# Kernel tuning notes

Measured on AMD Instinct MI355X. Metric: run time of the kernel, lower is better.

Reference implementation:

```python
import jax, jax.numpy as jnp
import numpy as np


def setup_inputs() -> dict:
    key = jax.random.key(0)
    k1, k2, k3, k4 = jax.random.split(key, 4)
    B, C, H, W = 4, 512, 64, 64
    K = 20
    Cp = C // 4  # 128, proj_feat output channels
    feat = jax.random.normal(k1, (B, C, H, W), dtype=jnp.float32)
    cam = jax.random.uniform(k2, (B, K, H, W), dtype=jnp.float32)
    # 1x1 conv == linear over channel dim; store kernel as [Cout, Cin]
    w_proj = jax.random.normal(k3, (Cp, C), dtype=jnp.float32) * (1.0 / np.sqrt(C))
    b_proj = jax.random.normal(k4, (Cp,), dtype=jnp.float32) * 0.01
    return {"feat": feat, "cam": cam, "w_proj": w_proj, "b_proj": b_proj}


def reference(feat, cam, w_proj, b_proj):
    B, C, H, W = feat.shape
    K = cam.shape[1]
    N = H * W
    cam_detach = jax.lax.stop_gradient(cam)
    # proj_feat: 1x1 conv -> [B, N, C//4] token layout (matches view+transpose)
    feat_proj = jnp.einsum('bchw,oc->bhwo', feat, w_proj) + b_proj
    feat_proj = feat_proj.reshape(B, N, -1)                      # [B, N, Cp]
    cam_reshape = cam_detach.reshape(B, K, N)                    # [B, K, N]
    class_term = jnp.einsum('bkn,bnd->bkd', cam_reshape, feat_proj)  # [B, K, Cp]
    # unscaled self-attention over N pixels
    pixel_sim = jnp.einsum('bnd,bmd->bnm', feat_proj, feat_proj)     # [B, N, N]
    pixel_sim = jax.nn.softmax(pixel_sim, axis=-1)
    pixel_term = jnp.einsum('bnm,bmd->bnd', pixel_sim, feat_proj)    # [B, N, Cp]
    aug_cam = jnp.einsum('bkd,bnd->bkn', class_term, pixel_term)     # [B, K, N]
    return cam + aug_cam.reshape(B, K, H, W)
```

## Files before the change

kernel.cpp:

```cpp
#include <hip/hip_runtime.h>
#include <hip/hip_bf16.h>
#include <math.h>

#define NB 4
#define NC 512
#define NN 4096
#define NK 20
#define NCP 128
#define SPLIT 4
#define CHUNK (NN / SPLIT)
#define NTILES (CHUNK / 64)

typedef __bf16 bf16x8 __attribute__((ext_vector_type(8)));
typedef float f32x4 __attribute__((ext_vector_type(4)));
typedef float f32x16 __attribute__((ext_vector_type(16)));
typedef short short8 __attribute__((ext_vector_type(8)));
typedef unsigned int uint4v __attribute__((ext_vector_type(4)));

static __device__ __forceinline__ unsigned short f2bf(float f) {
    unsigned int u = __builtin_bit_cast(unsigned int, f);
    unsigned int r = (u + 0x7FFFu + ((u >> 16) & 1u)) >> 16;
    return (unsigned short)r;
}
static __device__ __forceinline__ float bf2f(unsigned short h) {
    unsigned int u = ((unsigned int)h) << 16;
    return __builtin_bit_cast(float, u);
}
static __device__ __forceinline__ bf16x8 ldbf8(const unsigned short* p) {
    return __builtin_bit_cast(bf16x8, *reinterpret_cast<const short8*>(p));
}
static __device__ __forceinline__ void gld16(const unsigned short* g, unsigned short* l) {
    __builtin_amdgcn_global_load_lds(
        (const __attribute__((address_space(1))) unsigned int*)g,
        (__attribute__((address_space(3))) unsigned int*)l, 16, 0, 0);
}
static __device__ __forceinline__ unsigned int cvtpk(float lo, float hi) {
    unsigned int r;
    asm("v_cvt_pk_bf16_f32 %0, %1, %2" : "=v"(r) : "v"(lo), "v"(hi));
    return r;
}

#define MFMA16(a, b, c) __builtin_amdgcn_mfma_f32_16x16x32_bf16(a, b, c, 0, 0, 0)
#define MFMA32(a, b, c) __builtin_amdgcn_mfma_f32_32x32x16_bf16(a, b, c, 0, 0, 0)
#define SCHED0() __builtin_amdgcn_sched_barrier(0)
#define BAR() do { SCHED0(); __builtin_amdgcn_s_barrier(); SCHED0(); } while (0)

__global__ __launch_bounds__(256) void proj_kernel(
    const float* __restrict__ feat, const float* __restrict__ w,
    const float* __restrict__ bias, unsigned short* __restrict__ fp,
    unsigned short* __restrict__ fpT, float* __restrict__ ctg)
{
    const int b = blockIdx.y;
    const int n0 = blockIdx.x * 32;
    const int tid = threadIdx.x;
    const int wid = tid >> 6;
    const int lane = tid & 63;
    const int lg = lane >> 4, lr = lane & 15;

    if (blockIdx.x == 0 && blockIdx.y == 0) {
        #pragma unroll
        for (int i = 0; i < (NB * NK * NCP) / 256; ++i)
            ctg[i * 256 + tid] = 0.f;
    }

    __shared__ unsigned short lds_f[2][32][40];

    const float* featb = feat + (size_t)b * NC * NN;

    f32x4 acc[2][2];
    #pragma unroll
    for (int i = 0; i < 2; ++i)
        #pragma unroll
        for (int j = 0; j < 2; ++j) acc[i][j] = (f32x4){0.f, 0.f, 0.f, 0.f};

    const int cc = tid >> 3, q = tid & 7;
    float4 pre = *reinterpret_cast<const float4*>(&featb[(size_t)cc * NN + n0 + q * 4]);

    for (int c0 = 0; c0 < NC; c0 += 32) {
        const int cur = (c0 >> 5) & 1;
        lds_f[cur][q * 4 + 0][cc] = f2bf(pre.x);
        lds_f[cur][q * 4 + 1][cc] = f2bf(pre.y);
        lds_f[cur][q * 4 + 2][cc] = f2bf(pre.z);
        lds_f[cur][q * 4 + 3][cc] = f2bf(pre.w);
        __syncthreads();
        if (c0 + 32 < NC)
            pre = *reinterpret_cast<const float4*>(
                &featb[(size_t)(c0 + 32 + cc) * NN + n0 + q * 4]);
        bf16x8 afr[2];
        #pragma unroll
        for (int dt = 0; dt < 2; ++dt) {
            const float4* wr = reinterpret_cast<const float4*>(
                w + (size_t)(wid * 32 + dt * 16 + lr) * NC + c0 + lg * 8);
            float4 w0 = wr[0], w1 = wr[1];
            short8 a;
            a[0] = (short)f2bf(w0.x); a[1] = (short)f2bf(w0.y);
            a[2] = (short)f2bf(w0.z); a[3] = (short)f2bf(w0.w);
            a[4] = (short)f2bf(w1.x); a[5] = (short)f2bf(w1.y);
            a[6] = (short)f2bf(w1.z); a[7] = (short)f2bf(w1.w);
            afr[dt] = __builtin_bit_cast(bf16x8, a);
        }
        #pragma unroll
        for (int n1 = 0; n1 < 2; ++n1) {
            bf16x8 bfr = ldbf8(&lds_f[cur][n1 * 16 + lr][lg * 8]);
            #pragma unroll
            for (int dt = 0; dt < 2; ++dt)
                acc[dt][n1] = MFMA16(afr[dt], bfr, acc[dt][n1]);
        }
    }
    #pragma unroll
    for (int dt = 0; dt < 2; ++dt)
        #pragma unroll
        for (int n1 = 0; n1 < 2; ++n1)
            #pragma unroll
            for (int i = 0; i < 4; ++i) {
                int d = wid * 32 + dt * 16 + lg * 4 + i;
                int n = n0 + n1 * 16 + lr;
                unsigned short h = f2bf(acc[dt][n1][i] + bias[d]);
                fp[((size_t)b * NN + n) * NCP + d] = h;
                fpT[((size_t)b * NCP + d) * NN + n] = h;
            }
}

__global__ __launch_bounds__(256, 2) void attn_partial_kernel(
    const unsigned short* __restrict__ fp, const unsigned short* __restrict__ fpT,
    const float* __restrict__ cam, float* __restrict__ ctg,
    unsigned short* __restrict__ po, float* __restrict__ mbuf, float* __restrict__ lbuf)
{
    const int b = blockIdx.z;
    const int sidx = blockIdx.y;
    const int tid = threadIdx.x;
    const int wid = tid >> 6;
    const int lane = tid & 63;
    const int l31 = lane & 31, hi = lane >> 5;
    const int q0 = blockIdx.x * 128 + wid * 32;
    const int kvbase = sidx * CHUNK;

    __shared__ unsigned short kt[2][64 * 128];
    __shared__ unsigned short vt[2][64 * 128];
    __shared__ float cam_lds[CHUNK];

    const unsigned short* fpb  = fp  + (size_t)b * NN * NCP;
    const unsigned short* fpTb = fpT + (size_t)b * NCP * NN;

    const bool doCT = (blockIdx.x < NK);
    const int pd = tid & 63;
    const int qtr = tid >> 6;
    float ctx = 0.f, cty = 0.f;

    if (doCT) {
        const float* camb = cam + ((size_t)b * NK + blockIdx.x) * NN + kvbase;
        *reinterpret_cast<float4*>(&cam_lds[tid * 4]) =
            *reinterpret_cast<const float4*>(&camb[tid * 4]);
    }

    int offK[4], offV[4];
    #pragma unroll
    for (int i = 0; i < 4; ++i) {
        int oc = i * 256 + tid;
        int rk = oc >> 4, ck = oc & 15;
        offK[i] = rk * NCP + ((ck ^ (rk & 15)) << 3);
        int rowp = oc >> 4, cv = oc & 15;
        int cg = cv ^ (rowp & 15);
        int d = rowp * 2 + (cg >> 3), kvc = cg & 7;
        offV[i] = d * NN + (kvc << 3);
    }

    bf16x8 qf[8];
    #pragma unroll
    for (int kk = 0; kk < 8; ++kk)
        qf[kk] = ldbf8(&fpb[(size_t)(q0 + l31) * NCP + kk * 16 + hi * 8]);

    f32x16 o[4];
    #pragma unroll
    for (int dt = 0; dt < 4; ++dt)
        #pragma unroll
        for (int j = 0; j < 16; ++j) o[dt][j] = 0.f;
    float m_i = -INFINITY, l_i = 0.f;

    {
        const unsigned short* k0 = fpb + (size_t)kvbase * NCP;
        const unsigned short* v0 = fpTb + kvbase;
        #pragma unroll
        for (int i = 0; i < 4; ++i) {
            gld16(k0 + offK[i], &kt[0][(i * 256 + wid * 64) * 8]);
            gld16(v0 + offV[i], &vt[0][(i * 256 + wid * 64) * 8]);
        }
    }
    SCHED0();
    __syncthreads();

    for (int t = 0; t < NTILES; ++t) {
        const int cur = t & 1;
        if (t + 1 < NTILES) {
            const unsigned short* knext = fpb + (size_t)(kvbase + (t + 1) * 64) * NCP;
            const unsigned short* vnext = fpTb + kvbase + (t + 1) * 64;
            #pragma unroll
            for (int i = 0; i < 4; ++i) {
                gld16(knext + offK[i], &kt[cur ^ 1][(i * 256 + wid * 64) * 8]);
                gld16(vnext + offV[i], &vt[cur ^ 1][(i * 256 + wid * 64) * 8]);
            }
        }
        SCHED0();
        const unsigned short* ktc = &kt[cur][0];
        f32x16 s[2];
        #pragma unroll
        for (int g = 0; g < 2; ++g)
            #pragma unroll
            for (int j = 0; j < 16; ++j) s[g][j] = 0.f;
        __builtin_amdgcn_s_setprio(1);
        #pragma unroll
        for (int kk = 0; kk < 8; ++kk) {
            #pragma unroll
            for (int g = 0; g < 2; ++g) {
                int row = g * 32 + l31;
                bf16x8 kf = ldbf8(&ktc[row * 128 + (((kk * 2 + hi) ^ (row & 15)) << 3)]);
                s[g] = MFMA32(kf, qf[kk], s[g]);
            }
        }
        __builtin_amdgcn_s_setprio(0);
        float pmax = s[0][0];
        #pragma unroll
        for (int g = 0; g < 2; ++g)
            #pragma unroll
            for (int j = 0; j < 16; ++j) pmax = fmaxf(pmax, s[g][j]);
        pmax = fmaxf(pmax, __shfl_xor(pmax, 32));
        if (!__all(pmax - m_i <= 8.f)) {
            float mnew = fmaxf(m_i, pmax);
            float sc = __expf(m_i - mnew);
            l_i *= sc;
            #pragma unroll
            for (int dt = 0; dt < 4; ++dt)
                #pragma unroll
                for (int j = 0; j < 16; ++j) o[dt][j] *= sc;
            m_i = mnew;
        }
        float sum = 0.f;
        #pragma unroll
        for (int g = 0; g < 2; ++g)
            #pragma unroll
            for (int j = 0; j < 16; ++j) {
                float e = __expf(s[g][j] - m_i);
                s[g][j] = e;
                sum += e;
            }
        sum += __shfl_xor(sum, 32);
        l_i += sum;
        unsigned int wk[2][8];
        #pragma unroll
        for (int g = 0; g < 2; ++g)
            #pragma unroll
            for (int m = 0; m < 8; ++m)
                wk[g][m] = cvtpk(s[g][2 * m], s[g][2 * m + 1]);
        bf16x8 pf[4];
        #pragma unroll
        for (int g = 0; g < 2; ++g)
            #pragma unroll
            for (int sub = 0; sub < 2; ++sub) {
                unsigned int A0 = wk[g][4 * sub],     B0 = wk[g][4 * sub + 2];
                unsigned int A1 = wk[g][4 * sub + 1], B1 = wk[g][4 * sub + 3];
                asm("v_permlane32_swap_b32 %0, %1" : "+v"(A0), "+v"(B0));
                asm("v_permlane32_swap_b32 %0, %1" : "+v"(A1), "+v"(B1));
                uint4v u;
                u[0] = A0; u[1] = A1; u[2] = B0; u[3] = B1;
                pf[2 * g + sub] = __builtin_bit_cast(bf16x8, u);
            }
        const unsigned short* vtc = &vt[cur][0];
        __builtin_amdgcn_s_setprio(1);
        #pragma unroll
        for (int c2 = 0; c2 < 4; ++c2) {
            #pragma unroll
            for (int dt = 0; dt < 4; ++dt) {
                int row32 = dt * 32 + l31;
                int rowp = row32 >> 1;
                int chunk = (row32 & 1) * 8 + c2 * 2 + hi;
                bf16x8 vf = ldbf8(&vtc[rowp * 128 + ((chunk ^ (rowp & 15)) << 3)]);
                o[dt] = MFMA32(vf, pf[c2], o[dt]);
            }
        }
        __builtin_amdgcn_s_setprio(0);
        if (doCT) {
            float cf[16];
            const float4* cl = reinterpret_cast<const float4*>(&cam_lds[t * 64 + qtr * 16]);
            #pragma unroll
            for (int v4 = 0; v4 < 4; ++v4) {
                float4 c4 = cl[v4];
                cf[v4 * 4 + 0] = c4.x; cf[v4 * 4 + 1] = c4.y;
                cf[v4 * 4 + 2] = c4.z; cf[v4 * 4 + 3] = c4.w;
            }
            const int c8 = pd >> 2, de = (pd * 2) & 7;
            #pragma unroll
            for (int n = 0; n < 16; ++n) {
                int rown = qtr * 16 + n;
                unsigned int v = *reinterpret_cast<const unsigned int*>(
                    &ktc[rown * 128 + ((c8 ^ (rown & 15)) << 3) + de]);
                ctx += cf[n] * bf2f((unsigned short)(v & 0xffff));
                cty += cf[n] * bf2f((unsigned short)(v >> 16));
            }
        }
        SCHED0();
        asm volatile("s_waitcnt vmcnt(0)" ::: "memory");
        BAR();
    }
    const size_t pbase = (size_t)(b * SPLIT + sidx) * NN + q0;
    const size_t rowoff = (pbase + l31) * NCP;
    #pragma unroll
    for (int dt = 0; dt < 4; ++dt)
        #pragma unroll
        for (int qd = 0; qd < 4; ++qd) {
            unsigned int u0 = cvtpk(o[dt][qd * 4 + 0], o[dt][qd * 4 + 1]);
            unsigned int u1 = cvtpk(o[dt][qd * 4 + 2], o[dt][qd * 4 + 3]);
            *reinterpret_cast<uint2*>(&po[rowoff + dt * 32 + qd * 8 + hi * 4]) =
                make_uint2(u0, u1);
        }
    if (hi == 0) {
        mbuf[pbase + l31] = m_i;
        lbuf[pbase + l31] = l_i;
    }
    if (doCT) {
        float* ctp = &ctg[((size_t)b * NK + blockIdx.x) * NCP + pd * 2];
        atomicAdd(ctp, ctx);
        atomicAdd(ctp + 1, cty);
    }
}

__global__ __launch_bounds__(256) void aug_kernel(
    const float* __restrict__ cam, const float* __restrict__ ct,
    const unsigned short* __restrict__ po, const float* __restrict__ mbuf,
    const float* __restrict__ lbuf, float* __restrict__ out)
{
    const int b = blockIdx.y;
    const int tid = threadIdx.x, wid = tid >> 6, lane = tid & 63;
    const int lg = lane >> 4, lr = lane & 15;
    const int n0 = blockIdx.x * 64 + wid * 16;
    const int row = n0 + lr;
    const float* ctb = ct + (size_t)b * NK * NCP;

    float m_s[SPLIT], l_s[SPLIT];
    #pragma unroll
    for (int s = 0; s < SPLIT; ++s) {
        m_s[s] = mbuf[(size_t)(b * SPLIT + s) * NN + row];
        l_s[s] = lbuf[(size_t)(b * SPLIT + s) * NN + row];
    }
    uint4v pv[4][SPLIT];
    #pragma unroll
    for (int kk = 0; kk < 4; ++kk)
        #pragma unroll
        for (int s = 0; s < SPLIT; ++s)
            pv[kk][s] = *reinterpret_cast<const uint4v*>(
                &po[((size_t)(b * SPLIT + s) * NN + row) * NCP + kk * 32 + lg * 8]);

    float M = -INFINITY;
    #pragma unroll
    for (int s = 0; s < SPLIT; ++s) M = fmaxf(M, m_s[s]);
    float L = 0.f, wgt[SPLIT];
    #pragma unroll
    for (int s = 0; s < SPLIT; ++s) { wgt[s] = __expf(m_s[s] - M); L += wgt[s] * l_s[s]; }
    const float inv = 1.f / L;
    #pragma unroll
    for (int s = 0; s < SPLIT; ++s) wgt[s] *= inv;

    f32x4 acc[2];
    acc[0] = (f32x4){0.f, 0.f, 0.f, 0.f};
    acc[1] = (f32x4){0.f, 0.f, 0.f, 0.f};
    #pragma unroll
    for (int kk = 0; kk < 4; ++kk) {
        float mg[8];
        #pragma unroll
        for (int j = 0; j < 8; ++j) mg[j] = 0.f;
        #pragma unroll
        for (int s = 0; s < SPLIT; ++s) {
            uint4v v = pv[kk][s];
            #pragma unroll
            for (int j = 0; j < 4; ++j) {
                mg[2 * j]     += wgt[s] * bf2f((unsigned short)(v[j] & 0xffff));
                mg[2 * j + 1] += wgt[s] * bf2f((unsigned short)(v[j] >> 16));
            }
        }
        uint4v au;
        #pragma unroll
        for (int j = 0; j < 4; ++j) au[j] = cvtpk(mg[2 * j], mg[2 * j + 1]);
        bf16x8 af = __builtin_bit_cast(bf16x8, au);
        #pragma unroll
        for (int c = 0; c < 2; ++c) {
            int k = c * 16 + lr;
            short8 bv;
            if (k < NK) {
                const float* cr = &ctb[(size_t)k * NCP + kk * 32 + lg * 8];
                #pragma unroll
                for (int j = 0; j < 8; ++j) bv[j] = (short)f2bf(cr[j]);
            } else {
                #pragma unroll
                for (int j = 0; j < 8; ++j) bv[j] = 0;
            }
            acc[c] = MFMA16(af, __builtin_bit_cast(bf16x8, bv), acc[c]);
        }
    }
    #pragma unroll
    for (int c = 0; c < 2; ++c) {
        int k = c * 16 + lr;
        if (k < NK) {
            #pragma unroll
            for (int i = 0; i < 4; ++i) {
                size_t off = ((size_t)b * NK + k) * NN + n0 + lg * 4 + i;
                out[off] = cam[off] + acc[c][i];
            }
        }
    }
}

extern "C" void kernel_launch(void* const* d_in, const int* in_sizes, int n_in,
                              void* d_out, int out_size, void* d_ws, size_t ws_size,
                              hipStream_t stream) {
    const float* feat = (const float*)d_in[0];
    const float* cam  = (const float*)d_in[1];
    const float* wpr  = (const float*)d_in[2];
    const float* bpr  = (const float*)d_in[3];
    float* out = (float*)d_out;

    const size_t MB = 1024 * 1024;
    char* ws = (char*)d_ws;
    unsigned short* fp  = (unsigned short*)(ws);
    unsigned short* fpT = (unsigned short*)(ws + 4 * MB);
    float* ct           = (float*)(ws + 12 * MB);
    unsigned short* po  = (unsigned short*)(ws + 13 * MB);
    float* mbuf         = (float*)(ws + 30 * MB);
    float* lbuf         = (float*)(ws + 31 * MB);

    proj_kernel<<<dim3(NN / 32, NB), 256, 0, stream>>>(feat, wpr, bpr, fp, fpT, ct);
    attn_partial_kernel<<<dim3(NN / 128, SPLIT, NB), 256, 0, stream>>>(
        fp, fpT, cam, ct, po, mbuf, lbuf);
    aug_kernel<<<dim3(NN / 64, NB), 256, 0, stream>>>(cam, ct, po, mbuf, lbuf, out);
}
```

Baseline: 82.74 us.

## Use 32-row KV tiles with triple-buffered LDS prefetch two tiles ahead

Halves the KV tile size to 32 keys and switches from double to triple buffering in LDS, so loads for tile t+2 are issued while tile t is computed, with partial vmcnt waits. The V swizzle layout is adjusted for the narrower tile, and the cam load is issued as a register load before staging. The aim is deeper latency hiding and lower LDS footprint per buffer. The cost is twice as many barriers and softmax max/rescale steps per key, and less MFMA work between syncs.

```diff
diff --git a/kernel.cpp b/kernel.cpp
--- a/kernel.cpp
+++ b/kernel.cpp
@@ -9,7 +9,8 @@
 #define NCP 128
 #define SPLIT 4
 #define CHUNK (NN / SPLIT)
-#define NTILES (CHUNK / 64)
+#define KVB 32
+#define NTILES (CHUNK / KVB)
 
 typedef __bf16 bf16x8 __attribute__((ext_vector_type(8)));
 typedef float f32x4 __attribute__((ext_vector_type(4)));
@@ -135,8 +136,8 @@
     const int q0 = blockIdx.x * 128 + wid * 32;
     const int kvbase = sidx * CHUNK;
 
-    __shared__ unsigned short kt[2][64 * 128];
-    __shared__ unsigned short vt[2][64 * 128];
+    __shared__ unsigned short kt[3][KVB * 128];
+    __shared__ unsigned short vt[3][64 * 64];
     __shared__ float cam_lds[CHUNK];
 
     const unsigned short* fpb  = fp  + (size_t)b * NN * NCP;
@@ -147,22 +148,22 @@
     const int qtr = tid >> 6;
     float ctx = 0.f, cty = 0.f;
 
-    if (doCT) {
-        const float* camb = cam + ((size_t)b * NK + blockIdx.x) * NN + kvbase;
-        *reinterpret_cast<float4*>(&cam_lds[tid * 4]) =
-            *reinterpret_cast<const float4*>(&camb[tid * 4]);
-    }
-
-    int offK[4], offV[4];
-    #pragma unroll
-    for (int i = 0; i < 4; ++i) {
+    int offK[2], offV[2];
+    #pragma unroll
+    for (int i = 0; i < 2; ++i) {
         int oc = i * 256 + tid;
         int rk = oc >> 4, ck = oc & 15;
         offK[i] = rk * NCP + ((ck ^ (rk & 15)) << 3);
-        int rowp = oc >> 4, cv = oc & 15;
-        int cg = cv ^ (rowp & 15);
-        int d = rowp * 2 + (cg >> 3), kvc = cg & 7;
+        int rowp = oc >> 3, cv = oc & 7;
+        int cg = cv ^ (rowp & 7);
+        int d = rowp * 2 + (cg >> 2), kvc = cg & 3;
         offV[i] = d * NN + (kvc << 3);
+    }
+
+    float4 camv;
+    if (doCT) {
+        const float* camb = cam + ((size_t)b * NK + blockIdx.x) * NN + kvbase;
+        camv = *reinterpret_cast<const float4*>(&camb[tid * 4]);
     }
 
     bf16x8 qf[8];
@@ -177,52 +178,30 @@
         for (int j = 0; j < 16; ++j) o[dt][j] = 0.f;
     float m_i = -INFINITY, l_i = 0.f;
 
-    {
-        const unsigned short* k0 = fpb + (size_t)kvbase * NCP;
-        const unsigned short* v0 = fpTb + kvbase;
-        #pragma unroll
-        for (int i = 0; i < 4; ++i) {
-            gld16(k0 + offK[i], &kt[0][(i * 256 + wid * 64) * 8]);
-            gld16(v0 + offV[i], &vt[0][(i * 256 + wid * 64) * 8]);
-        }
-    }
-    SCHED0();
-    __syncthreads();
-
-    for (int t = 0; t < NTILES; ++t) {
-        const int cur = t & 1;
-        if (t + 1 < NTILES) {
-            const unsigned short* knext = fpb + (size_t)(kvbase + (t + 1) * 64) * NCP;
-            const unsigned short* vnext = fpTb + kvbase + (t + 1) * 64;
-            #pragma unroll
-            for (int i = 0; i < 4; ++i) {
-                gld16(knext + offK[i], &kt[cur ^ 1][(i * 256 + wid * 64) * 8]);
-                gld16(vnext + offV[i], &vt[cur ^ 1][(i * 256 + wid * 64) * 8]);
-            }
-        }
-        SCHED0();
-        const unsigned short* ktc = &kt[cur][0];
-        f32x16 s[2];
-        #pragma unroll
-        for (int g = 0; g < 2; ++g)
-            #pragma unroll
-            for (int j = 0; j < 16; ++j) s[g][j] = 0.f;
+    auto stage = [&](int tt, int bi) {
+        const unsigned short* kn = fpb + (size_t)(kvbase + tt * KVB) * NCP;
+        const unsigned short* vn = fpTb + kvbase + tt * KVB;
+        #pragma unroll
+        for (int i = 0; i < 2; ++i) {
+            gld16(kn + offK[i], &kt[bi][(i * 256 + wid * 64) * 8]);
+            gld16(vn + offV[i], &vt[bi][(i * 256 + wid * 64) * 8]);
+        }
+    };
+
+    auto compute_tile = [&](const unsigned short* ktc, const unsigned short* vtc, int t) {
+        f32x16 s;
+        #pragma unroll
+        for (int j = 0; j < 16; ++j) s[j] = 0.f;
         __builtin_amdgcn_s_setprio(1);
         #pragma unroll
         for (int kk = 0; kk < 8; ++kk) {
-            #pragma unroll
-            for (int g = 0; g < 2; ++g) {
-                int row = g * 32 + l31;
-                bf16x8 kf = ldbf8(&ktc[row * 128 + (((kk * 2 + hi) ^ (row & 15)) << 3)]);
-                s[g] = MFMA32(kf, qf[kk], s[g]);
-            }
+            bf16x8 kf = ldbf8(&ktc[l31 * 128 + (((kk * 2 + hi) ^ (l31 & 15)) << 3)]);
+            s = MFMA32(kf, qf[kk], s);
         }
         __builtin_amdgcn_s_setprio(0);
-        float pmax = s[0][0];
-        #pragma unroll
-        for (int g = 0; g < 2; ++g)
-            #pragma unroll
-            for (int j = 0; j < 16; ++j) pmax = fmaxf(pmax, s[g][j]);
+        float pmax = s[0];
+        #pragma unroll
+        for (int j = 1; j < 16; ++j) pmax = fmaxf(pmax, s[j]);
         pmax = fmaxf(pmax, __shfl_xor(pmax, 32));
         if (!__all(pmax - m_i <= 8.f)) {
             float mnew = fmaxf(m_i, pmax);
@@ -236,71 +215,83 @@
         }
         float sum = 0.f;
         #pragma unroll
-        for (int g = 0; g < 2; ++g)
-            #pragma unroll
-            for (int j = 0; j < 16; ++j) {
-                float e = __expf(s[g][j] - m_i);
-                s[g][j] = e;
-                sum += e;
-            }
+        for (int j = 0; j < 16; ++j) {
+            float e = __expf(s[j] - m_i);
+            s[j] = e;
+            sum += e;
+        }
         sum += __shfl_xor(sum, 32);
         l_i += sum;
-        unsigned int wk[2][8];
-        #pragma unroll
-        for (int g = 0; g < 2; ++g)
-            #pragma unroll
-            for (int m = 0; m < 8; ++m)
-                wk[g][m] = cvtpk(s[g][2 * m], s[g][2 * m + 1]);
-        bf16x8 pf[4];
-        #pragma unroll
-        for (int g = 0; g < 2; ++g)
-            #pragma unroll
-            for (int sub = 0; sub < 2; ++sub) {
-                unsigned int A0 = wk[g][4 * sub],     B0 = wk[g][4 * sub + 2];
-                unsigned int A1 = wk[g][4 * sub + 1], B1 = wk[g][4 * sub + 3];
-                asm("v_permlane32_swap_b32 %0, %1" : "+v"(A0), "+v"(B0));
-                asm("v_permlane32_swap_b32 %0, %1" : "+v"(A1), "+v"(B1));
-                uint4v u;
-                u[0] = A0; u[1] = A1; u[2] = B0; u[3] = B1;
-                pf[2 * g + sub] = __builtin_bit_cast(bf16x8, u);
-            }
-        const unsigned short* vtc = &vt[cur][0];
+        unsigned int wkk[8];
+        #pragma unroll
+        for (int m = 0; m < 8; ++m)
+            wkk[m] = cvtpk(s[2 * m], s[2 * m + 1]);
+        bf16x8 pf[2];
+        #pragma unroll
+        for (int sub = 0; sub < 2; ++sub) {
+            unsigned int A0 = wkk[4 * sub],     B0 = wkk[4 * sub + 2];
+            unsigned int A1 = wkk[4 * sub + 1], B1 = wkk[4 * sub + 3];
+            asm("v_permlane32_swap_b32 %0, %1" : "+v"(A0), "+v"(B0));
+            asm("v_permlane32_swap_b32 %0, %1" : "+v"(A1), "+v"(B1));
+            uint4v u;
+            u[0] = A0; u[1] = A1; u[2] = B0; u[3] = B1;
+            pf[sub] = __builtin_bit_cast(bf16x8, u);
+        }
         __builtin_amdgcn_s_setprio(1);
         #pragma unroll
-        for (int c2 = 0; c2 < 4; ++c2) {
+        for (int c2 = 0; c2 < 2; ++c2) {
             #pragma unroll
             for (int dt = 0; dt < 4; ++dt) {
                 int row32 = dt * 32 + l31;
                 int rowp = row32 >> 1;
-                int chunk = (row32 & 1) * 8 + c2 * 2 + hi;
-                bf16x8 vf = ldbf8(&vtc[rowp * 128 + ((chunk ^ (rowp & 15)) << 3)]);
+                int chunk = (row32 & 1) * 4 + c2 * 2 + hi;
+                bf16x8 vf = ldbf8(&vtc[rowp * 64 + ((chunk ^ (rowp & 7)) << 3)]);
                 o[dt] = MFMA32(vf, pf[c2], o[dt]);
             }
         }
         __builtin_amdgcn_s_setprio(0);
         if (doCT) {
-            float cf[16];
-            const float4* cl = reinterpret_cast<const float4*>(&cam_lds[t * 64 + qtr * 16]);
-            #pragma unroll
-            for (int v4 = 0; v4 < 4; ++v4) {
-                float4 c4 = cl[v4];
-                cf[v4 * 4 + 0] = c4.x; cf[v4 * 4 + 1] = c4.y;
-                cf[v4 * 4 + 2] = c4.z; cf[v4 * 4 + 3] = c4.w;
-            }
+            const float4* cl = reinterpret_cast<const float4*>(&cam_lds[t * KVB + qtr * 8]);
+            float4 c0 = cl[0], c1 = cl[1];
+            float cf[8] = {c0.x, c0.y, c0.z, c0.w, c1.x, c1.y, c1.z, c1.w};
             const int c8 = pd >> 2, de = (pd * 2) & 7;
             #pragma unroll
-            for (int n = 0; n < 16; ++n) {
-                int rown = qtr * 16 + n;
+            for (int n = 0; n < 8; ++n) {
+                int rown = qtr * 8 + n;
                 unsigned int v = *reinterpret_cast<const unsigned int*>(
                     &ktc[rown * 128 + ((c8 ^ (rown & 15)) << 3) + de]);
                 ctx += cf[n] * bf2f((unsigned short)(v & 0xffff));
                 cty += cf[n] * bf2f((unsigned short)(v >> 16));
             }
         }
+    };
+
+    stage(0, 0);
+    stage(1, 1);
+    if (doCT)
+        *reinterpret_cast<float4*>(&cam_lds[tid * 4]) = camv;
+    SCHED0();
+    asm volatile("s_waitcnt vmcnt(4) lgkmcnt(0)" ::: "memory");
+    BAR();
+
+    int bc = 0;
+    for (int t = 0; t < NTILES - 2; ++t) {
+        int b2 = bc + 2; if (b2 >= 3) b2 -= 3;
+        stage(t + 2, b2);
         SCHED0();
-        asm volatile("s_waitcnt vmcnt(0)" ::: "memory");
+        compute_tile(&kt[bc][0], &vt[bc][0], t);
+        SCHED0();
+        asm volatile("s_waitcnt vmcnt(4)" ::: "memory");
         BAR();
-    }
+        bc = (bc == 2) ? 0 : bc + 1;
+    }
+    compute_tile(&kt[bc][0], &vt[bc][0], NTILES - 2);
+    SCHED0();
+    asm volatile("s_waitcnt vmcnt(0)" ::: "memory");
+    BAR();
+    bc = (bc == 2) ? 0 : bc + 1;
+    compute_tile(&kt[bc][0], &vt[bc][0], NTILES - 1);
+
     const size_t pbase = (size_t)(b * SPLIT + sidx) * NN + q0;
     const size_t rowoff = (pbase + l31) * NCP;
     #pragma unroll
```

After: 87.43 us. 1.06x slower.
